# Performance work log

Measured on AMD Instinct MI355X. Metric: run time of the kernel, lower is better.

The kernel has to match this reference:

```python
import jax, jax.numpy as jnp
import numpy as np

B, M, D, H = 2, 2048, 1024, 16
DH = D // H            # 64 head dim
FF = 2624              # GeGLU intermediate size
EPS = 1e-5
ROPE_BASE = 10000.0


def _layernorm(x, g, b):
    mu = jnp.mean(x, axis=-1, keepdims=True)
    var = jnp.mean(jnp.square(x - mu), axis=-1, keepdims=True)
    return (x - mu) * jax.lax.rsqrt(var + EPS) * g + b


def _rope_cos_sin(m, dh):
    # HF-style: inv_freq over even dims; only first dh/2 entries are used by apply_rope
    inv_freq = 1.0 / (ROPE_BASE ** (jnp.arange(0, dh, 2, dtype=jnp.float32) / dh))  # [dh/2]
    ang = jnp.arange(m, dtype=jnp.float32)[:, None] * inv_freq[None, :]             # [M, dh/2]
    return jnp.cos(ang), jnp.sin(ang)


def _apply_rope(x, c, s):
    # x: [B,H,M,dh]; c,s: [M,dh/2] broadcast over B,H. Half-split (non-interleaved) rotation.
    x1, x2 = jnp.split(x, 2, axis=-1)
    return jnp.concatenate([x1 * c - x2 * s, x1 * s + x2 * c], axis=-1)


def setup_inputs() -> dict:
    key = jax.random.key(0)
    ks = jax.random.split(key, 6)
    w = lambda k, shape: (jax.random.normal(k, shape, jnp.float32) * 0.02)
    return {
        "hidden_states": jax.random.normal(ks[0], (B, M, D), jnp.float32),
        "attention_mask": jnp.ones((B, M), jnp.int32),
        "ln1_g": jnp.ones((D,), jnp.float32),
        "ln1_b": jnp.zeros((D,), jnp.float32),
        "Wqkv_w": w(ks[1], (3 * D, D)),
        "Wqkv_b": jnp.zeros((3 * D,), jnp.float32),
        "Wo_w": w(ks[2], (D, D)),
        "ln2_g": jnp.ones((D,), jnp.float32),
        "ln2_b": jnp.zeros((D,), jnp.float32),
        "Wi_w": w(ks[3], (2 * FF, D)),
        "Wmlp_o_w": w(ks[4], (D, FF)),
    }


def reference(hidden_states, attention_mask, ln1_g, ln1_b, Wqkv_w, Wqkv_b, Wo_w,
              ln2_g, ln2_b, Wi_w, Wmlp_o_w):
    x = hidden_states                                    # [B,M,D]
    xn = _layernorm(x, ln1_g, ln1_b)
    qkv = xn @ Wqkv_w.T + Wqkv_b                         # [B,M,3D]
    qkv = qkv.reshape(B, M, 3, H, DH).transpose(0, 3, 1, 2, 4)  # [B,H,M,3,dh]
    q, k, v = qkv[..., 0, :], qkv[..., 1, :], qkv[..., 2, :]    # each [B,H,M,dh]

    c, s = _rope_cos_sin(M, DH)                          # [M, dh/2]
    q = _apply_rope(q, c, s)
    k = _apply_rope(k, c, s)

    scale = 1.0 / np.sqrt(DH)
    scores = jnp.einsum("bhmd,bhnd->bhmn", q, k) * scale  # [B,H,M,M]
    keep = (attention_mask > 0)[:, None, None, :]         # [B,1,1,M] padding mask on keys
    scores = jnp.where(keep, scores, -jnp.inf)
    p = jax.nn.softmax(scores, axis=-1)
    o = jnp.einsum("bhmn,bhnd->bhmd", p, v)               # [B,H,M,dh]

    attn_out = o.transpose(0, 2, 1, 3).reshape(B, M, D)
    x = x + attn_out @ Wo_w.T

    # ModernBERT GeGLU MLP: input, gate = Wi(x).chunk(2); Wo(gelu(input) * gate)
    xn2 = _layernorm(x, ln2_g, ln2_b)
    hg = xn2 @ Wi_w.T                                     # [B,M,2*FF]
    h_in, h_gate = jnp.split(hg, 2, axis=-1)
    x = x + (jax.nn.gelu(h_in) * h_gate) @ Wmlp_o_w.T
    return x
```

## Files before the change

### kernel.cpp

```cpp
#include <hip/hip_runtime.h>
#include <cstdint>
#include <cstddef>

using u16 = unsigned short;
using u32 = uint32_t;

typedef __attribute__((ext_vector_type(8))) short short8;
typedef __attribute__((ext_vector_type(4))) float floatx4;

#define DEVFN static __device__ __forceinline__

#define QSCALE 0.18033688011112042f

DEVFN u16 f2bf(float f) {
  u32 u = __float_as_uint(f);
  return (u16)((u + 0x7fffu + ((u >> 16) & 1u)) >> 16);
}

DEVFN float b2f(u16 u) { return __uint_as_float(((u32)u) << 16); }

DEVFN void async_load16(const void* g, const void* lds) {
  __builtin_amdgcn_global_load_lds(
      (const __attribute__((address_space(1))) u32*)(uintptr_t)g,
      (__attribute__((address_space(3))) u32*)(u32)(uintptr_t)lds,
      16, 0, 0);
}

DEVFN void cvt4(const float* __restrict__ src, u16* __restrict__ dst, int i) {
  const float4 v = ((const float4*)src)[i];
  ushort4 o;
  o.x = f2bf(v.x); o.y = f2bf(v.y); o.z = f2bf(v.z); o.w = f2bf(v.w);
  ((ushort4*)dst)[i] = o;
}

__global__ __launch_bounds__(256)
void prep_k(const float* __restrict__ Wqkv, const float* __restrict__ Wo,
            const float* __restrict__ Wi, const float* __restrict__ Wmlp,
            const float* __restrict__ hidden, const float* __restrict__ ln1g,
            const float* __restrict__ ln1b,
            u16* __restrict__ wqkv_bf, u16* __restrict__ wo_bf,
            u16* __restrict__ wi_bf, u16* __restrict__ wmlp_bf,
            float* __restrict__ ct, float* __restrict__ st, u16* __restrict__ xn) {
  const int bid = blockIdx.x;
  const int tid = threadIdx.x;
  __shared__ float red[8];
  if (bid < 256) {
    const int i = bid * 256 + tid;
    const int m = i >> 5, f = i & 31;
    const float inv = exp2f((float)f * -0.41524101186092025f);
    const float ang = (float)m * inv;
    ct[i] = cosf(ang);
    st[i] = sinf(ang);
  } else if (bid < 3328) {
    cvt4(Wqkv, wqkv_bf, (bid - 256) * 256 + tid);
  } else if (bid < 4352) {
    cvt4(Wo, wo_bf, (bid - 3328) * 256 + tid);
  } else if (bid < 9600) {
    const int i = (bid - 4352) * 256 + tid;
    const int i4 = i * 4;
    const int p = i4 >> 10, kc = i4 & 1023;
    const int g = p >> 5, c = p & 31;
    const int srow = (c < 16) ? (g * 16 + c) : (2624 + g * 16 + (c - 16));
    const float4 v = *(const float4*)(Wi + (size_t)srow * 1024 + kc);
    ushort4 o;
    o.x = f2bf(v.x); o.y = f2bf(v.y); o.z = f2bf(v.z); o.w = f2bf(v.w);
    ((ushort4*)wi_bf)[i] = o;
  } else if (bid < 12224) {
    cvt4(Wmlp, wmlp_bf, (bid - 9600) * 256 + tid);
  } else {
    const int row = bid - 12224;
    const float4 v = ((const float4*)(hidden + (size_t)row * 1024))[tid];
    float s = v.x + v.y + v.z + v.w;
    float ss = v.x * v.x + v.y * v.y + v.z * v.z + v.w * v.w;
#pragma unroll
    for (int d = 32; d > 0; d >>= 1) {
      s += __shfl_xor(s, d);
      ss += __shfl_xor(ss, d);
    }
    const int wave = tid >> 6;
    if ((tid & 63) == 0) { red[wave] = s; red[4 + wave] = ss; }
    __syncthreads();
    s = red[0] + red[1] + red[2] + red[3];
    ss = red[4] + red[5] + red[6] + red[7];
    const float mu = s * (1.f / 1024.f);
    const float var = ss * (1.f / 1024.f) - mu * mu;
    const float rr = rsqrtf(var + 1e-5f);
    const float4 gv = ((const float4*)ln1g)[tid];
    const float4 bv = ((const float4*)ln1b)[tid];
    u16* orow = xn + (size_t)row * 1024 + tid * 4;
    orow[0] = f2bf((v.x - mu) * rr * gv.x + bv.x);
    orow[1] = f2bf((v.y - mu) * rr * gv.y + bv.y);
    orow[2] = f2bf((v.z - mu) * rr * gv.z + bv.z);
    orow[3] = f2bf((v.w - mu) * rr * gv.w + bv.w);
  }
}

__global__ __launch_bounds__(256)
void red_ln_k(const float* __restrict__ resid, const u16* __restrict__ p0,
              const u16* __restrict__ p1, const u16* __restrict__ p2,
              const float* __restrict__ g, const float* __restrict__ bb,
              float* __restrict__ outx, u16* __restrict__ outn) {
  const int row = blockIdx.x;
  const int tid = threadIdx.x;
  const size_t base = (size_t)row * 1024;
  const float4 h = ((const float4*)(resid + base))[tid];
  const ushort4 a = ((const ushort4*)(p0 + base))[tid];
  const ushort4 c = ((const ushort4*)(p1 + base))[tid];
  const ushort4 d = ((const ushort4*)(p2 + base))[tid];
  float4 v;
  v.x = h.x + b2f(a.x) + b2f(c.x) + b2f(d.x);
  v.y = h.y + b2f(a.y) + b2f(c.y) + b2f(d.y);
  v.z = h.z + b2f(a.z) + b2f(c.z) + b2f(d.z);
  v.w = h.w + b2f(a.w) + b2f(c.w) + b2f(d.w);
  float s = v.x + v.y + v.z + v.w;
  float ss = v.x * v.x + v.y * v.y + v.z * v.z + v.w * v.w;
#pragma unroll
  for (int dd = 32; dd > 0; dd >>= 1) {
    s += __shfl_xor(s, dd);
    ss += __shfl_xor(ss, dd);
  }
  __shared__ float red[8];
  const int wave = tid >> 6;
  if ((tid & 63) == 0) { red[wave] = s; red[4 + wave] = ss; }
  __syncthreads();
  s = red[0] + red[1] + red[2] + red[3];
  ss = red[4] + red[5] + red[6] + red[7];
  const float mu = s * (1.f / 1024.f);
  const float var = ss * (1.f / 1024.f) - mu * mu;
  const float rr = rsqrtf(var + 1e-5f);
  ((float4*)(outx + base))[tid] = v;
  const float4 gv = ((const float4*)g)[tid];
  const float4 bv = ((const float4*)bb)[tid];
  u16* orow = outn + base + tid * 4;
  orow[0] = f2bf((v.x - mu) * rr * gv.x + bv.x);
  orow[1] = f2bf((v.y - mu) * rr * gv.y + bv.y);
  orow[2] = f2bf((v.z - mu) * rr * gv.z + bv.z);
  orow[3] = f2bf((v.w - mu) * rr * gv.w + bv.w);
}

__global__ void red_add_k(float* __restrict__ out, const u16* __restrict__ p0,
                          const u16* __restrict__ p1, const u16* __restrict__ p2,
                          const u16* __restrict__ p3) {
  const int i = blockIdx.x * 256 + threadIdx.x;
  float4 v = ((const float4*)out)[i];
  const ushort4 a = ((const ushort4*)p0)[i];
  const ushort4 c = ((const ushort4*)p1)[i];
  const ushort4 d = ((const ushort4*)p2)[i];
  const ushort4 e = ((const ushort4*)p3)[i];
  v.x += b2f(a.x) + b2f(c.x) + b2f(d.x) + b2f(e.x);
  v.y += b2f(a.y) + b2f(c.y) + b2f(d.y) + b2f(e.y);
  v.z += b2f(a.z) + b2f(c.z) + b2f(d.z) + b2f(e.z);
  v.w += b2f(a.w) + b2f(c.w) + b2f(d.w) + b2f(e.w);
  ((float4*)out)[i] = v;
}

DEVFN void swizzle_tile(int NT, int& tn, int& tm) {
  const int tpx = gridDim.x >> 3;
  const int p = blockIdx.x;
  const int lid = (p & 7) * tpx + (p >> 3);
  const int band = lid / (8 * NT);
  const int rem = lid - band * 8 * NT;
  tn = (rem >> 3) * 128;
  tm = (band * 8 + (rem & 7)) * 128;
}

struct EpiArgs {
  const float* bias;
  u16* q; u16* kk; u16* vt;
  u16* outbf;
  const float* ct; const float* st;
};

template <int EPI>
__global__ __launch_bounds__(256, 3)
void gemm_k(const u16* __restrict__ A, const u16* __restrict__ B, int K, int NT,
            EpiArgs ea) {
  __shared__ __align__(16) u16 sA[128 * 32];
  __shared__ __align__(16) u16 sB[128 * 32];
  int tn, tm;
  swizzle_tile(NT, tn, tm);
  const int tid = threadIdx.x;
  const int wave = tid >> 6, lane = tid & 63;
  const int quad = lane >> 4, l15 = lane & 15;
  const int wm = (wave >> 1) * 64, wn = (wave & 1) * 64;

  floatx4 acc[4][4];
#pragma unroll
  for (int i = 0; i < 4; ++i)
#pragma unroll
    for (int j = 0; j < 4; ++j) acc[i][j] = (floatx4){0.f, 0.f, 0.f, 0.f};

  const int srow = lane >> 2;
  const int skc = (lane & 3) * 8;
  const u16* sAr = sA + (wm + l15) * 32 + quad * 8;
  const u16* sBr = sB + (wn + l15) * 32 + quad * 8;

  for (int k0 = 0; k0 < K; k0 += 32) {
#pragma unroll
    for (int j = 0; j < 2; ++j) {
      const int q = wave * 2 + j;
      const int row = q * 16 + srow;
      async_load16(A + (size_t)(tm + row) * K + (k0 + skc), (const char*)sA + q * 1024);
      async_load16(B + (size_t)(tn + row) * K + (k0 + skc), (const char*)sB + q * 1024);
    }
    __syncthreads();
    short8 af[4], bfr[4];
#pragma unroll
    for (int t = 0; t < 4; ++t) af[t] = *(const short8*)(sAr + t * 512);
#pragma unroll
    for (int t = 0; t < 4; ++t) bfr[t] = *(const short8*)(sBr + t * 512);
#pragma unroll
    for (int ti = 0; ti < 4; ++ti)
#pragma unroll
      for (int tj = 0; tj < 4; ++tj)
        acc[ti][tj] = __builtin_amdgcn_mfma_f32_16x16x32_bf16(af[ti], bfr[tj], acc[ti][tj], 0, 0, 0);
    __syncthreads();
  }

  if constexpr (EPI == 0) {
    const int col0 = tn + wn;
    const int t = col0 >> 10;
    const int h = (col0 & 1023) >> 6;
    if (t == 2) {
#pragma unroll
      for (int ti = 0; ti < 4; ++ti)
#pragma unroll
        for (int r = 0; r < 4; ++r) {
          const int row = tm + wm + ti * 16 + quad * 4 + r;
          const int b = row >> 11, m = row & 2047;
          const int mp = (m & ~31) | ((m & 15) << 1) | ((m >> 4) & 1);
#pragma unroll
          for (int tj = 0; tj < 4; ++tj) {
            const int dh = tj * 16 + l15;
            const float v = acc[ti][tj][r] + ea.bias[col0 + dh];
            ea.vt[((size_t)((b * 16 + h) * 64 + dh)) * 2048 + mp] = f2bf(v);
          }
        }
    } else {
      u16* dst = (t == 0) ? ea.q : ea.kk;
      const float qs = (t == 0) ? QSCALE : 1.f;
#pragma unroll
      for (int ti = 0; ti < 4; ++ti)
#pragma unroll
        for (int r = 0; r < 4; ++r) {
          const int row = tm + wm + ti * 16 + quad * 4 + r;
          const int b = row >> 11, m = row & 2047;
          u16* drow = dst + ((size_t)(b * 16 + h) * 2048 + m) * 64;
#pragma unroll
          for (int tj = 0; tj < 2; ++tj) {
            const int i = tj * 16 + l15;
            const float x1 = acc[ti][tj][r] + ea.bias[col0 + i];
            const float x2 = acc[ti][tj + 2][r] + ea.bias[col0 + 32 + i];
            const float cs = ea.ct[m * 32 + i];
            const float sn = ea.st[m * 32 + i];
            drow[i] = f2bf((x1 * cs - x2 * sn) * qs);
            drow[32 + i] = f2bf((x1 * sn + x2 * cs) * qs);
          }
        }
    }
  } else {
#pragma unroll
    for (int ti = 0; ti < 4; ++ti)
#pragma unroll
      for (int r = 0; r < 4; ++r) {
        const int row = tm + wm + ti * 16 + quad * 4 + r;
#pragma unroll
        for (int u = 0; u < 2; ++u) {
          const float hin = acc[ti][2 * u][r];
          const float hg = acc[ti][2 * u + 1][r];
          const int a = (((tn + wn) >> 5) + u) * 16 + l15;
          const float t2 = hin + 0.044715f * hin * hin * hin;
          const float e = __builtin_amdgcn_exp2f(t2 * -2.302114768f);
          const float gl = hin * __builtin_amdgcn_rcpf(1.f + e);
          ea.outbf[(size_t)row * 2624 + a] = f2bf(gl * hg);
        }
      }
  }
}

__global__ __launch_bounds__(256, 3)
void gemm_sk4(const u16* __restrict__ A, const u16* __restrict__ B, int K, int NT,
              int kps1, int zsw, int kps2,
              u16* __restrict__ p0, u16* __restrict__ p1,
              u16* __restrict__ p2, u16* __restrict__ p3) {
  __shared__ __align__(16) u16 sA[128 * 32];
  __shared__ __align__(16) u16 sB[128 * 32];
  int tn, tm;
  swizzle_tile(NT, tn, tm);
  const int z = blockIdx.y;
  int kofs, kps;
  if (z < zsw) { kofs = z * kps1; kps = kps1; }
  else { kofs = zsw * kps1 + (z - zsw) * kps2; kps = kps2; }
  const int tid = threadIdx.x;
  const int wave = tid >> 6, lane = tid & 63;
  const int quad = lane >> 4, l15 = lane & 15;
  const int wm = (wave >> 1) * 64, wn = (wave & 1) * 64;

  floatx4 acc[4][4];
#pragma unroll
  for (int i = 0; i < 4; ++i)
#pragma unroll
    for (int j = 0; j < 4; ++j) acc[i][j] = (floatx4){0.f, 0.f, 0.f, 0.f};

  const int srow = lane >> 2;
  const int skc = (lane & 3) * 8;
  const u16* sAr = sA + (wm + l15) * 32 + quad * 8;
  const u16* sBr = sB + (wn + l15) * 32 + quad * 8;

  for (int k0 = 0; k0 < kps; k0 += 32) {
    const int kk = kofs + k0;
#pragma unroll
    for (int j = 0; j < 2; ++j) {
      const int q = wave * 2 + j;
      const int row = q * 16 + srow;
      async_load16(A + (size_t)(tm + row) * K + (kk + skc), (const char*)sA + q * 1024);
      async_load16(B + (size_t)(tn + row) * K + (kk + skc), (const char*)sB + q * 1024);
    }
    __syncthreads();
    short8 af[4], bfr[4];
#pragma unroll
    for (int t = 0; t < 4; ++t) af[t] = *(const short8*)(sAr + t * 512);
#pragma unroll
    for (int t = 0; t < 4; ++t) bfr[t] = *(const short8*)(sBr + t * 512);
#pragma unroll
    for (int ti = 0; ti < 4; ++ti)
#pragma unroll
      for (int tj = 0; tj < 4; ++tj)
        acc[ti][tj] = __builtin_amdgcn_mfma_f32_16x16x32_bf16(af[ti], bfr[tj], acc[ti][tj], 0, 0, 0);
    __syncthreads();
  }

  u16* part = (z == 0) ? p0 : (z == 1) ? p1 : (z == 2) ? p2 : p3;
#pragma unroll
  for (int ti = 0; ti < 4; ++ti)
#pragma unroll
    for (int r = 0; r < 4; ++r) {
      const int row = tm + wm + ti * 16 + quad * 4 + r;
#pragma unroll
      for (int tj = 0; tj < 4; ++tj)
        part[(size_t)row * 1024 + tn + wn + tj * 16 + l15] = f2bf(acc[ti][tj][r]);
    }
}

DEVFN void attn_stage(const u16* __restrict__ kg, size_t bhbase_k, int key0,
                      int wave, int lane, const u16* sK) {
#pragma unroll
  for (int j = 0; j < 4; ++j) {
    const int qi = wave * 4 + j;
    const int chunk = qi >> 1, half = qi & 1;
    const int row = half * 64 + lane;
    async_load16(kg + bhbase_k + (size_t)(key0 + row) * 64 + chunk * 8,
                 (const char*)sK + qi * 1024);
  }
}

__global__ __launch_bounds__(256, 2)
void attn_k(const u16* __restrict__ qg, const u16* __restrict__ kg,
            const u16* __restrict__ vtg, const int* __restrict__ mask,
            u16* __restrict__ outg) {
  __shared__ __align__(16) u16 sK2[2][8192];
  __shared__ __align__(16) u16 sP[8 * 16 * 40];
  const int bh = blockIdx.y;
  const int b = bh >> 4, h = bh & 15;
  const int q0 = blockIdx.x * 128;
  const int tid = threadIdx.x;
  const int wave = tid >> 6, lane = tid & 63;
  const int quad = lane >> 4, l15 = lane & 15;
  const size_t bhk = (size_t)bh * 2048 * 64;
  const size_t bhv = (size_t)bh * 64 * 2048;

  short8 aq[2][2];
#pragma unroll
  for (int g = 0; g < 2; ++g) {
    const u16* qptr = qg + ((size_t)bh * 2048 + q0 + wave * 32 + g * 16 + l15) * 64 + quad * 8;
    aq[g][0] = *(const short8*)qptr;
    aq[g][1] = *(const short8*)(qptr + 32);
  }

  floatx4 o[2][4];
#pragma unroll
  for (int g = 0; g < 2; ++g)
#pragma unroll
    for (int t = 0; t < 4; ++t) o[g][t] = (floatx4){0.f, 0.f, 0.f, 0.f};
  float li[2][4] = {{0.f, 0.f, 0.f, 0.f}, {0.f, 0.f, 0.f, 0.f}};
  const floatx4 z4 = {0.f, 0.f, 0.f, 0.f};

  const u16* vbase = vtg + bhv + (size_t)l15 * 2048 + quad * 8;

  float mbc[8];
#pragma unroll
  for (int tj = 0; tj < 8; ++tj)
    mbc[tj] = (mask[b * 2048 + tj * 16 + l15] > 0) ? 0.f : -1e30f;

  attn_stage(kg, bhk, 0, wave, lane, sK2[0]);
  __syncthreads();

  int buf = 0;
  for (int kt = 0; kt < 16; ++kt) {
    const u16* sK = sK2[buf];
    const int key0 = kt * 128;
    float mbn[8];
    if (kt < 15) {
      attn_stage(kg, bhk, key0 + 128, wave, lane, sK2[buf ^ 1]);
#pragma unroll
      for (int tj = 0; tj < 8; ++tj)
        mbn[tj] = (mask[b * 2048 + key0 + 128 + tj * 16 + l15] > 0) ? 0.f : -1e30f;
    }

    floatx4 sacc[2][8];
    __builtin_amdgcn_s_setprio(1);
#pragma unroll
    for (int tj = 0; tj < 8; ++tj) {
      const short8 b0 = *(const short8*)(sK + quad * 1024 + (tj * 16 + l15) * 8);
      const short8 b1 = *(const short8*)(sK + (4 + quad) * 1024 + (tj * 16 + l15) * 8);
      sacc[0][tj] = __builtin_amdgcn_mfma_f32_16x16x32_bf16(aq[0][0], b0, z4, 0, 0, 0);
      sacc[0][tj] = __builtin_amdgcn_mfma_f32_16x16x32_bf16(aq[0][1], b1, sacc[0][tj], 0, 0, 0);
      sacc[1][tj] = __builtin_amdgcn_mfma_f32_16x16x32_bf16(aq[1][0], b0, z4, 0, 0, 0);
      sacc[1][tj] = __builtin_amdgcn_mfma_f32_16x16x32_bf16(aq[1][1], b1, sacc[1][tj], 0, 0, 0);
    }
    __builtin_amdgcn_s_setprio(0);

    short8 bv[4][4];
    const u16* vb = vbase + key0;
#pragma unroll
    for (int t = 0; t < 4; ++t) bv[0][t] = *(const short8*)(vb + (size_t)t * 32768);
#pragma unroll
    for (int t = 0; t < 4; ++t) bv[1][t] = *(const short8*)(vb + (size_t)t * 32768 + 32);

    const float msum = mbc[0] + mbc[1] + mbc[2] + mbc[3] + mbc[4] + mbc[5] + mbc[6] + mbc[7];
    if (__all(msum == 0.f)) {
#pragma unroll
      for (int g = 0; g < 2; ++g)
#pragma unroll
        for (int r = 0; r < 4; ++r) {
          float sum = li[g][r];
#pragma unroll
          for (int tj = 0; tj < 8; ++tj) {
            const float p = __builtin_amdgcn_exp2f(sacc[g][tj][r]);
            sacc[g][tj][r] = p;
            sum += p;
          }
          li[g][r] = sum;
        }
    } else {
#pragma unroll
      for (int g = 0; g < 2; ++g)
#pragma unroll
        for (int r = 0; r < 4; ++r) {
          float sum = li[g][r];
#pragma unroll
          for (int tj = 0; tj < 8; ++tj) {
            const float p = __builtin_amdgcn_exp2f(sacc[g][tj][r] + mbc[tj]);
            sacc[g][tj][r] = p;
            sum += p;
          }
          li[g][r] = sum;
        }
    }

#pragma unroll
    for (int c = 0; c < 4; ++c) {
#pragma unroll
      for (int g = 0; g < 2; ++g) {
        u32* pw32 = (u32*)sP + (wave * 2 + g) * 320;
#pragma unroll
        for (int r = 0; r < 4; ++r) {
          const u32 lo = __float_as_uint(sacc[g][c * 2][r]) + 0x8000u;
          const u32 hi = __float_as_uint(sacc[g][c * 2 + 1][r]) + 0x8000u;
          pw32[(quad * 4 + r) * 20 + l15] = __builtin_amdgcn_perm(hi, lo, 0x07060302);
        }
      }
      asm volatile("s_waitcnt lgkmcnt(0)" ::: "memory");
      short8 ap[2];
#pragma unroll
      for (int g = 0; g < 2; ++g)
        ap[g] = *(const short8*)(sP + (wave * 2 + g) * 640 + l15 * 40 + quad * 8);
      if (c == 0) {
#pragma unroll
        for (int t = 0; t < 4; ++t) bv[2][t] = *(const short8*)(vb + (size_t)t * 32768 + 64);
      }
      if (c == 1) {
#pragma unroll
        for (int t = 0; t < 4; ++t) bv[3][t] = *(const short8*)(vb + (size_t)t * 32768 + 96);
      }
      __builtin_amdgcn_s_setprio(1);
#pragma unroll
      for (int tj2 = 0; tj2 < 4; ++tj2) {
        o[0][tj2] = __builtin_amdgcn_mfma_f32_16x16x32_bf16(ap[0], bv[c][tj2], o[0][tj2], 0, 0, 0);
        o[1][tj2] = __builtin_amdgcn_mfma_f32_16x16x32_bf16(ap[1], bv[c][tj2], o[1][tj2], 0, 0, 0);
      }
      __builtin_amdgcn_s_setprio(0);
    }
    __syncthreads();
#pragma unroll
    for (int tj = 0; tj < 8; ++tj) mbc[tj] = mbn[tj];
    buf ^= 1;
  }

#pragma unroll
  for (int g = 0; g < 2; ++g)
#pragma unroll
    for (int r = 0; r < 4; ++r) {
      float s = li[g][r];
      s += __shfl_xor(s, 1);
      s += __shfl_xor(s, 2);
      s += __shfl_xor(s, 4);
      s += __shfl_xor(s, 8);
      li[g][r] = 1.f / s;
    }

#pragma unroll
  for (int g = 0; g < 2; ++g)
#pragma unroll
    for (int tj = 0; tj < 4; ++tj)
#pragma unroll
      for (int r = 0; r < 4; ++r) {
        const int m = q0 + wave * 32 + g * 16 + quad * 4 + r;
        outg[((size_t)b * 2048 + m) * 1024 + h * 64 + tj * 16 + l15] =
            f2bf(o[g][tj][r] * li[g][r]);
      }
}

static const size_t OFF_WQKV = 0;
static const size_t OFF_WO   = 6291456;
static const size_t OFF_WI   = 8388608;
static const size_t OFF_WMLP = 19136512;
static const size_t OFF_XN   = 24510464;
static const size_t OFF_Q    = 32899072;
static const size_t OFF_K    = 41287680;
static const size_t OFF_VT   = 49676288;
static const size_t OFF_ATT  = 58064896;
static const size_t OFF_ROPE = OFF_ATT;
static const size_t WS_NEED  = 66453504;

extern "C" void kernel_launch(void* const* d_in, const int* in_sizes, int n_in,
                              void* d_out, int out_size, void* d_ws, size_t ws_size,
                              hipStream_t stream) {
  (void)in_sizes; (void)n_in; (void)out_size;
  if (ws_size < WS_NEED) return;

  const float* hidden = (const float*)d_in[0];
  const int*   mask   = (const int*)d_in[1];
  const float* ln1g   = (const float*)d_in[2];
  const float* ln1b   = (const float*)d_in[3];
  const float* Wqkv   = (const float*)d_in[4];
  const float* Wqkvb  = (const float*)d_in[5];
  const float* Wo     = (const float*)d_in[6];
  const float* ln2g   = (const float*)d_in[7];
  const float* ln2b   = (const float*)d_in[8];
  const float* Wi     = (const float*)d_in[9];
  const float* Wmlp   = (const float*)d_in[10];
  float* out = (float*)d_out;
  char* ws = (char*)d_ws;

  u16* wqkv_bf = (u16*)(ws + OFF_WQKV);
  u16* wo_bf   = (u16*)(ws + OFF_WO);
  u16* wi_bf   = (u16*)(ws + OFF_WI);
  u16* wmlp_bf = (u16*)(ws + OFF_WMLP);
  u16* xn      = (u16*)(ws + OFF_XN);
  u16* qb      = (u16*)(ws + OFF_Q);
  u16* kb      = (u16*)(ws + OFF_K);
  u16* vtb     = (u16*)(ws + OFF_VT);
  u16* att     = (u16*)(ws + OFF_ATT);
  u16* act     = (u16*)(ws + OFF_Q);
  float* ct    = (float*)(ws + OFF_ROPE);
  float* st    = (float*)(ws + OFF_ROPE + 262144);
  u16* wp0     = (u16*)(ws + OFF_Q);
  u16* wp1     = (u16*)(ws + OFF_K);
  u16* wp2     = (u16*)(ws + OFF_VT);
  u16* mp0     = (u16*)(ws + OFF_XN);
  u16* mp1     = (u16*)(ws + OFF_ATT);
  u16* mp2     = (u16*)(ws + OFF_WI);
  u16* mp3     = (u16*)(ws + OFF_WQKV);

  prep_k<<<16320, 256, 0, stream>>>(Wqkv, Wo, Wi, Wmlp, hidden, ln1g, ln1b,
                                    wqkv_bf, wo_bf, wi_bf, wmlp_bf, ct, st, xn);

  EpiArgs e1 = {Wqkvb, qb, kb, vtb, nullptr, ct, st};
  gemm_k<0><<<768, 256, 0, stream>>>(xn, wqkv_bf, 1024, 24, e1);

  attn_k<<<dim3(16, 32), 256, 0, stream>>>(qb, kb, vtb, mask, att);

  gemm_sk4<<<dim3(256, 3), 256, 0, stream>>>(att, wo_bf, 1024, 8, 352, 2, 320,
                                             wp0, wp1, wp2, wp2);
  red_ln_k<<<4096, 256, 0, stream>>>(hidden, wp0, wp1, wp2, ln2g, ln2b, out, xn);

  EpiArgs e3 = {nullptr, nullptr, nullptr, nullptr, act, nullptr, nullptr};
  gemm_k<2><<<1312, 256, 0, stream>>>(xn, wi_bf, 1024, 41, e3);

  gemm_sk4<<<dim3(256, 4), 256, 0, stream>>>(act, wmlp_bf, 2624, 8, 672, 2, 640,
                                             mp0, mp1, mp2, mp3);
  red_add_k<<<4096, 256, 0, stream>>>(out, mp0, mp1, mp2, mp3);
}
```

Baseline: 366.6 us.

## Split attention over two key halves, stage V in LDS, add combine kernel

```diff
diff --git a/kernel.cpp b/kernel.cpp
--- a/kernel.cpp
+++ b/kernel.cpp
@@ -154,6 +154,27 @@
   ((float4*)out)[i] = v;
 }
 
+__global__ __launch_bounds__(256)
+void red_att_k(u16* __restrict__ att, const u16* __restrict__ p0,
+               const float* __restrict__ li0, const float* __restrict__ li1) {
+  const int i = blockIdx.x * 256 + threadIdx.x;
+  const int i4 = i * 4;
+  const int row = i4 >> 10;
+  const int col = i4 & 1023;
+  const int b = row >> 11, m = row & 2047;
+  const int h = col >> 6;
+  const int bhm = (b * 16 + h) * 2048 + m;
+  const float rl = 1.f / (li0[bhm] + li1[bhm]);
+  const ushort4 a = ((const ushort4*)p0)[i];
+  const ushort4 c = ((const ushort4*)att)[i];
+  ushort4 o;
+  o.x = f2bf((b2f(a.x) + b2f(c.x)) * rl);
+  o.y = f2bf((b2f(a.y) + b2f(c.y)) * rl);
+  o.z = f2bf((b2f(a.z) + b2f(c.z)) * rl);
+  o.w = f2bf((b2f(a.w) + b2f(c.w)) * rl);
+  ((ushort4*)att)[i] = o;
+}
+
 DEVFN void swizzle_tile(int NT, int& tn, int& tm) {
   const int tpx = gridDim.x >> 3;
   const int p = blockIdx.x;
@@ -342,27 +363,39 @@
     }
 }
 
-DEVFN void attn_stage(const u16* __restrict__ kg, size_t bhbase_k, int key0,
-                      int wave, int lane, const u16* sK) {
+DEVFN void attn_stage64(const u16* __restrict__ kg, const u16* __restrict__ vtg,
+                        size_t bhk, size_t bhv, int key0, int wave, int lane,
+                        const u16* sK, const u16* sV) {
 #pragma unroll
   for (int j = 0; j < 4; ++j) {
     const int qi = wave * 4 + j;
-    const int chunk = qi >> 1, half = qi & 1;
-    const int row = half * 64 + lane;
-    async_load16(kg + bhbase_k + (size_t)(key0 + row) * 64 + chunk * 8,
-                 (const char*)sK + qi * 1024);
-  }
-}
-
-__global__ __launch_bounds__(256, 2)
+    if (qi < 8) {
+      async_load16(kg + bhk + (size_t)(key0 + lane) * 64 + qi * 8,
+                   (const char*)sK + qi * 1024);
+    } else {
+      const int vi = qi - 8;
+      const int c = vi >> 2, kc = vi & 3;
+      async_load16(vtg + bhv + (size_t)lane * 2048 + key0 + c * 32 + kc * 8,
+                   (const char*)sV + vi * 1024);
+    }
+  }
+}
+
+__global__ __launch_bounds__(256, 3)
 void attn_k(const u16* __restrict__ qg, const u16* __restrict__ kg,
             const u16* __restrict__ vtg, const int* __restrict__ mask,
-            u16* __restrict__ outg) {
-  __shared__ __align__(16) u16 sK2[2][8192];
+            u16* __restrict__ p0g, u16* __restrict__ p1g,
+            float* __restrict__ li0, float* __restrict__ li1) {
+  __shared__ __align__(16) u16 sKV[2][8192];
   __shared__ __align__(16) u16 sP[8 * 16 * 40];
-  const int bh = blockIdx.y;
+  const int L = blockIdx.x;
+  const int xcd = L & 7, idx = L >> 3;
+  const int bh = (xcd << 2) | (idx >> 5);
+  const int local = idx & 31;
+  const int q0 = (local >> 1) * 128;
+  const int z = local & 1;
+  const int keyBase = z << 10;
   const int b = bh >> 4, h = bh & 15;
-  const int q0 = blockIdx.x * 128;
   const int tid = threadIdx.x;
   const int wave = tid >> 6, lane = tid & 63;
   const int quad = lane >> 4, l15 = lane & 15;
@@ -385,34 +418,34 @@
   float li[2][4] = {{0.f, 0.f, 0.f, 0.f}, {0.f, 0.f, 0.f, 0.f}};
   const floatx4 z4 = {0.f, 0.f, 0.f, 0.f};
 
-  const u16* vbase = vtg + bhv + (size_t)l15 * 2048 + quad * 8;
-
-  float mbc[8];
-#pragma unroll
-  for (int tj = 0; tj < 8; ++tj)
-    mbc[tj] = (mask[b * 2048 + tj * 16 + l15] > 0) ? 0.f : -1e30f;
-
-  attn_stage(kg, bhk, 0, wave, lane, sK2[0]);
+  float mbc[4];
+#pragma unroll
+  for (int tj = 0; tj < 4; ++tj)
+    mbc[tj] = (mask[b * 2048 + keyBase + tj * 16 + l15] > 0) ? 0.f : -1e30f;
+
+  attn_stage64(kg, vtg, bhk, bhv, keyBase, wave, lane, sKV[0], sKV[0] + 4096);
   __syncthreads();
 
   int buf = 0;
   for (int kt = 0; kt < 16; ++kt) {
-    const u16* sK = sK2[buf];
-    const int key0 = kt * 128;
-    float mbn[8];
+    const u16* sK = sKV[buf];
+    const u16* sV = sKV[buf] + 4096;
+    const int key0 = keyBase + kt * 64;
+    float mbn[4];
     if (kt < 15) {
-      attn_stage(kg, bhk, key0 + 128, wave, lane, sK2[buf ^ 1]);
-#pragma unroll
-      for (int tj = 0; tj < 8; ++tj)
-        mbn[tj] = (mask[b * 2048 + key0 + 128 + tj * 16 + l15] > 0) ? 0.f : -1e30f;
-    }
-
-    floatx4 sacc[2][8];
+      attn_stage64(kg, vtg, bhk, bhv, key0 + 64, wave, lane,
+                   sKV[buf ^ 1], sKV[buf ^ 1] + 4096);
+#pragma unroll
+      for (int tj = 0; tj < 4; ++tj)
+        mbn[tj] = (mask[b * 2048 + key0 + 64 + tj * 16 + l15] > 0) ? 0.f : -1e30f;
+    }
+
+    floatx4 sacc[2][4];
     __builtin_amdgcn_s_setprio(1);
 #pragma unroll
-    for (int tj = 0; tj < 8; ++tj) {
-      const short8 b0 = *(const short8*)(sK + quad * 1024 + (tj * 16 + l15) * 8);
-      const short8 b1 = *(const short8*)(sK + (4 + quad) * 1024 + (tj * 16 + l15) * 8);
+    for (int tj = 0; tj < 4; ++tj) {
+      const short8 b0 = *(const short8*)(sK + quad * 512 + (tj * 16 + l15) * 8);
+      const short8 b1 = *(const short8*)(sK + (4 + quad) * 512 + (tj * 16 + l15) * 8);
       sacc[0][tj] = __builtin_amdgcn_mfma_f32_16x16x32_bf16(aq[0][0], b0, z4, 0, 0, 0);
       sacc[0][tj] = __builtin_amdgcn_mfma_f32_16x16x32_bf16(aq[0][1], b1, sacc[0][tj], 0, 0, 0);
       sacc[1][tj] = __builtin_amdgcn_mfma_f32_16x16x32_bf16(aq[1][0], b0, z4, 0, 0, 0);
@@ -420,14 +453,7 @@
     }
     __builtin_amdgcn_s_setprio(0);
 
-    short8 bv[4][4];
-    const u16* vb = vbase + key0;
-#pragma unroll
-    for (int t = 0; t < 4; ++t) bv[0][t] = *(const short8*)(vb + (size_t)t * 32768);
-#pragma unroll
-    for (int t = 0; t < 4; ++t) bv[1][t] = *(const short8*)(vb + (size_t)t * 32768 + 32);
-
-    const float msum = mbc[0] + mbc[1] + mbc[2] + mbc[3] + mbc[4] + mbc[5] + mbc[6] + mbc[7];
+    const float msum = mbc[0] + mbc[1] + mbc[2] + mbc[3];
     if (__all(msum == 0.f)) {
 #pragma unroll
       for (int g = 0; g < 2; ++g)
@@ -435,7 +461,7 @@
         for (int r = 0; r < 4; ++r) {
           float sum = li[g][r];
 #pragma unroll
-          for (int tj = 0; tj < 8; ++tj) {
+          for (int tj = 0; tj < 4; ++tj) {
             const float p = __builtin_amdgcn_exp2f(sacc[g][tj][r]);
             sacc[g][tj][r] = p;
             sum += p;
@@ -449,7 +475,7 @@
         for (int r = 0; r < 4; ++r) {
           float sum = li[g][r];
 #pragma unroll
-          for (int tj = 0; tj < 8; ++tj) {
+          for (int tj = 0; tj < 4; ++tj) {
             const float p = __builtin_amdgcn_exp2f(sacc[g][tj][r] + mbc[tj]);
             sacc[g][tj][r] = p;
             sum += p;
@@ -459,7 +485,7 @@
     }
 
 #pragma unroll
-    for (int c = 0; c < 4; ++c) {
+    for (int c = 0; c < 2; ++c) {
 #pragma unroll
       for (int g = 0; g < 2; ++g) {
         u32* pw32 = (u32*)sP + (wave * 2 + g) * 320;
@@ -475,25 +501,18 @@
 #pragma unroll
       for (int g = 0; g < 2; ++g)
         ap[g] = *(const short8*)(sP + (wave * 2 + g) * 640 + l15 * 40 + quad * 8);
-      if (c == 0) {
-#pragma unroll
-        for (int t = 0; t < 4; ++t) bv[2][t] = *(const short8*)(vb + (size_t)t * 32768 + 64);
-      }
-      if (c == 1) {
-#pragma unroll
-        for (int t = 0; t < 4; ++t) bv[3][t] = *(const short8*)(vb + (size_t)t * 32768 + 96);
-      }
       __builtin_amdgcn_s_setprio(1);
 #pragma unroll
       for (int tj2 = 0; tj2 < 4; ++tj2) {
-        o[0][tj2] = __builtin_amdgcn_mfma_f32_16x16x32_bf16(ap[0], bv[c][tj2], o[0][tj2], 0, 0, 0);
-        o[1][tj2] = __builtin_amdgcn_mfma_f32_16x16x32_bf16(ap[1], bv[c][tj2], o[1][tj2], 0, 0, 0);
+        const short8 bv = *(const short8*)(sV + (c * 4 + quad) * 512 + (tj2 * 16 + l15) * 8);
+        o[0][tj2] = __builtin_amdgcn_mfma_f32_16x16x32_bf16(ap[0], bv, o[0][tj2], 0, 0, 0);
+        o[1][tj2] = __builtin_amdgcn_mfma_f32_16x16x32_bf16(ap[1], bv, o[1][tj2], 0, 0, 0);
       }
       __builtin_amdgcn_s_setprio(0);
     }
     __syncthreads();
 #pragma unroll
-    for (int tj = 0; tj < 8; ++tj) mbc[tj] = mbn[tj];
+    for (int tj = 0; tj < 4; ++tj) mbc[tj] = mbn[tj];
     buf ^= 1;
   }
 
@@ -506,18 +525,29 @@
       s += __shfl_xor(s, 2);
       s += __shfl_xor(s, 4);
       s += __shfl_xor(s, 8);
-      li[g][r] = 1.f / s;
-    }
-
-#pragma unroll
-  for (int g = 0; g < 2; ++g)
-#pragma unroll
-    for (int tj = 0; tj < 4; ++tj)
+      li[g][r] = s;
+    }
+
+  u16* pz = z ? p1g : p0g;
+  float* lz = z ? li1 : li0;
+  if (l15 == 0) {
+#pragma unroll
+    for (int g = 0; g < 2; ++g)
 #pragma unroll
       for (int r = 0; r < 4; ++r) {
         const int m = q0 + wave * 32 + g * 16 + quad * 4 + r;
-        outg[((size_t)b * 2048 + m) * 1024 + h * 64 + tj * 16 + l15] =
-            f2bf(o[g][tj][r] * li[g][r]);
+        lz[(size_t)bh * 2048 + m] = li[g][r];
+      }
+  }
+
+#pragma unroll
+  for (int g = 0; g < 2; ++g)
+#pragma unroll
+    for (int tj = 0; tj < 4; ++tj)
+#pragma unroll
+      for (int r = 0; r < 4; ++r) {
+        const int m = q0 + wave * 32 + g * 16 + quad * 4 + r;
+        pz[((size_t)b * 2048 + m) * 1024 + h * 64 + tj * 16 + l15] = f2bf(o[g][tj][r]);
       }
 }
 
@@ -565,6 +595,10 @@
   u16* act     = (u16*)(ws + OFF_Q);
   float* ct    = (float*)(ws + OFF_ROPE);
   float* st    = (float*)(ws + OFF_ROPE + 262144);
+  u16* ap0     = (u16*)(ws + OFF_XN);
+  u16* ap1     = (u16*)(ws + OFF_ATT);
+  float* li0   = (float*)(ws + OFF_WQKV);
+  float* li1   = (float*)(ws + OFF_WQKV + 262144);
   u16* wp0     = (u16*)(ws + OFF_Q);
   u16* wp1     = (u16*)(ws + OFF_K);
   u16* wp2     = (u16*)(ws + OFF_VT);
@@ -579,7 +613,8 @@
   EpiArgs e1 = {Wqkvb, qb, kb, vtb, nullptr, ct, st};
   gemm_k<0><<<768, 256, 0, stream>>>(xn, wqkv_bf, 1024, 24, e1);
 
-  attn_k<<<dim3(16, 32), 256, 0, stream>>>(qb, kb, vtb, mask, att);
+  attn_k<<<dim3(1024), 256, 0, stream>>>(qb, kb, vtb, mask, ap0, ap1, li0, li1);
+  red_att_k<<<4096, 256, 0, stream>>>(att, ap0, li0, li1);
 
   gemm_sk4<<<dim3(256, 3), 256, 0, stream>>>(att, wo_bf, 1024, 8, 352, 2, 320,
                                              wp0, wp1, wp2, wp2);
```

Result: faster. 351.1 us (-4.2%).
